# Performance work log

Hardware: AMD Instinct MI355X
Metric: run time of the kernel (lower is better)

## Reference

```python
import jax, jax.numpy as jnp
import numpy as np

NEG_SLOPE = 0.2
EPS = 1e-16


def gatv2_conv(x, src, dst, n_nodes, Wl, Wr, att, bias):
    """GATv2Conv, heads=1, add_self_loops handled by caller via src/dst.
    x: [N, Fin]; src/dst: [E] (message j->i means src=j, dst=i).
    Wl, Wr: [Fin, Fout]; att: [Fout]; bias: [Fout].
    """
    xl = x @ Wl  # [N, Fout] (source transform)
    xr = x @ Wr  # [N, Fout] (target transform)
    # per-edge attention logit: a^T LeakyReLU(xl[j] + xr[i])
    h = xl[src] + xr[dst]                      # [E, Fout]
    e = jax.nn.leaky_relu(h, NEG_SLOPE) @ att  # [E]
    # segment softmax over incoming edges of each dst node
    m = jax.ops.segment_max(e, dst, num_segments=n_nodes)   # [N]
    ex = jnp.exp(e - m[dst])                                 # [E]
    denom = jax.ops.segment_sum(ex, dst, num_segments=n_nodes)  # [N]
    alpha = ex / (denom[dst] + EPS)                          # [E]
    # scatter-aggregate weighted source messages
    out = jax.ops.segment_sum(alpha[:, None] * xl[src], dst, num_segments=n_nodes)
    return out + bias


def glorot(key, shape):
    lim = np.sqrt(6.0 / (shape[0] + shape[1]))
    return jax.random.uniform(key, shape, jnp.float32, -lim, lim)


def setup_inputs() -> dict:
    key = jax.random.key(0)
    ks = jax.random.split(key, 9)
    N, E, Fin, H, Fout = 50000, 800000, 128, 64, 2
    x = jax.random.normal(ks[0], (N, Fin), jnp.float32)
    edge_index = jax.random.randint(ks[1], (2, E), 0, N, jnp.int64)
    return {
        "x": x,
        "edge_index": edge_index,
        "Wl1": glorot(ks[2], (Fin, H)),
        "Wr1": glorot(ks[3], (Fin, H)),
        "att1": glorot(ks[4], (H, 1))[:, 0],
        "b1": jnp.zeros((H,), jnp.float32),
        "Wl2": glorot(ks[5], (H, Fout)),
        "Wr2": glorot(ks[6], (H, Fout)),
        "att2": glorot(ks[7], (Fout, 1))[:, 0],
        "b2": jnp.zeros((Fout,), jnp.float32),
    }


def reference(x, edge_index, Wl1, Wr1, att1, b1, Wl2, Wr2, att2, b2):
    n_nodes = x.shape[0]
    # PyG GATv2Conv adds self-loops by default
    loops = jnp.arange(n_nodes, dtype=edge_index.dtype)
    src = jnp.concatenate([edge_index[0], loops])
    dst = jnp.concatenate([edge_index[1], loops])
    # eval mode: dropout is identity; the initial relu/dropout result is dead code
    h = gatv2_conv(x, src, dst, n_nodes, Wl1, Wr1, att1, b1)
    out = gatv2_conv(h, src, dst, n_nodes, Wl2, Wr2, att2, b2)
    return out
```

## Files before the change

### kernel.cpp

```cpp
#include <hip/hip_runtime.h>
#include <math.h>

#define FIN 128
#define H 64
#define FOUT 2
#define NEG_SLOPE 0.2f
#define EPS 1e-16f

#define SCAN_CHUNK 2048

typedef __attribute__((ext_vector_type(8))) short s8v;
typedef __attribute__((ext_vector_type(4))) float f4v;

__device__ __forceinline__ void load_bs(const int* __restrict__ blocksum, int nscan,
                                        int* bs, int tid){
  if(tid < 64){
    int v = (tid < nscan)? blocksum[tid] : 0;
    int incl = v;
    #pragma unroll
    for(int o=1;o<64;o<<=1){ int u=__shfl_up(incl,o); if(tid>=o) incl+=u; }
    bs[tid] = incl - v;
  }
  __syncthreads();
}

__global__ void k_prep(int* __restrict__ deg, int N, int ZB,
                       const float* __restrict__ Wl, const float* __restrict__ Wr,
                       unsigned short* __restrict__ pWh, unsigned short* __restrict__ pWe){
  int b = blockIdx.x;
  if(b < ZB){
    int i = b*256 + threadIdx.x;
    if(i < N) deg[i] = 0;
    return;
  }
  int idx = (b - ZB)*256 + threadIdx.x;
  int lane = idx & 63;
  int ctk  = idx >> 6;
  int k0   = (ctk & 3) * 32;
  int ct   = ctk >> 2;
  int c    = ct*16 + (lane & 15);
  int kb   = k0 + (lane >> 4)*8;
  const float* Wp = (c < 64) ? (Wl + c) : (Wr + (c - 64));
  #pragma unroll
  for(int j=0;j<8;j++){
    float v = Wp[(size_t)(kb + j)*H];
    unsigned u = __float_as_uint(v);
    unsigned short hb = (unsigned short)(u >> 16);
    float hv = __uint_as_float(((unsigned)hb) << 16);
    float ev = v - hv;
    unsigned short eb = (unsigned short)(__float_as_uint(ev) >> 16);
    pWh[(size_t)idx*8 + j] = hb;
    pWe[(size_t)idx*8 + j] = eb;
  }
}

__global__ __launch_bounds__(256) void k_gemm_mfma(
    const float* __restrict__ x,
    const unsigned short* __restrict__ pWh, const unsigned short* __restrict__ pWe,
    float* __restrict__ xr, unsigned short* __restrict__ xlb, int N){
  int tid = threadIdx.x;
  int lane = tid & 63, wid = tid >> 6;
  int rowbase = blockIdx.x*64 + wid*16;
  int r = lane & 15, g = lane >> 4;

  int arow = rowbase + r; if(arow > N-1) arow = N-1;
  const float* xrow = x + (size_t)arow*FIN;
  int orow = rowbase + r;

  s8v xh[4], xe[4];
  #pragma unroll
  for(int k0=0;k0<4;k0++){
    float4 va = *(const float4*)(xrow + k0*32 + g*8);
    float4 vb = *(const float4*)(xrow + k0*32 + g*8 + 4);
    float xs_[8] = {va.x,va.y,va.z,va.w,vb.x,vb.y,vb.z,vb.w};
    #pragma unroll
    for(int j=0;j<8;j++){
      unsigned u = __float_as_uint(xs_[j]);
      unsigned short hb = (unsigned short)(u >> 16);
      xh[k0][j] = (short)hb;
      float ev = xs_[j] - __uint_as_float(((unsigned)hb) << 16);
      xe[k0][j] = (short)(unsigned short)(__float_as_uint(ev) >> 16);
    }
  }

  #pragma unroll 2
  for(int ct=0;ct<8;ct++){
    f4v a = (f4v){0.f,0.f,0.f,0.f};
    #pragma unroll
    for(int k0=0;k0<4;k0++){
      size_t boff = ((size_t)(ct*4 + k0)*64 + lane)*8;
      s8v wh = *(const s8v*)(pWh + boff);
      s8v we = *(const s8v*)(pWe + boff);
      a = __builtin_amdgcn_mfma_f32_16x16x32_bf16(wh, xh[k0], a, 0,0,0);
      a = __builtin_amdgcn_mfma_f32_16x16x32_bf16(wh, xe[k0], a, 0,0,0);
      a = __builtin_amdgcn_mfma_f32_16x16x32_bf16(we, xh[k0], a, 0,0,0);
    }
    if(orow < N){
      if(ct < 4){
        ushort4 pk;
        unsigned u0 = __float_as_uint(a[0]);
        unsigned u1 = __float_as_uint(a[1]);
        unsigned u2 = __float_as_uint(a[2]);
        unsigned u3 = __float_as_uint(a[3]);
        pk.x = (unsigned short)((u0 + 0x7FFF + ((u0>>16)&1)) >> 16);
        pk.y = (unsigned short)((u1 + 0x7FFF + ((u1>>16)&1)) >> 16);
        pk.z = (unsigned short)((u2 + 0x7FFF + ((u2>>16)&1)) >> 16);
        pk.w = (unsigned short)((u3 + 0x7FFF + ((u3>>16)&1)) >> 16);
        *(ushort4*)(xlb + (size_t)orow*H + ct*16 + g*4) = pk;
      } else {
        *(float4*)(xr + (size_t)orow*H + (ct-4)*16 + g*4) =
            make_float4(a[0],a[1],a[2],a[3]);
      }
    }
  }
}

__global__ void k_degree(const int* __restrict__ ei, int E, int Etot,
                         int* __restrict__ deg, int* __restrict__ rank){
  int i0 = (blockIdx.x*blockDim.x + threadIdx.x)*8;
  if(i0 >= Etot) return;
  if(i0 + 8 <= E && (E & 3) == 0){
    int4 da = *(const int4*)(ei + E + i0);
    int4 db = *(const int4*)(ei + E + i0 + 4);
    int r0 = atomicAdd(&deg[da.x],1);
    int r1 = atomicAdd(&deg[da.y],1);
    int r2 = atomicAdd(&deg[da.z],1);
    int r3 = atomicAdd(&deg[da.w],1);
    int r4 = atomicAdd(&deg[db.x],1);
    int r5 = atomicAdd(&deg[db.y],1);
    int r6 = atomicAdd(&deg[db.z],1);
    int r7 = atomicAdd(&deg[db.w],1);
    *(int4*)(rank + i0)     = make_int4(r0,r1,r2,r3);
    *(int4*)(rank + i0 + 4) = make_int4(r4,r5,r6,r7);
  } else if(i0 >= E && i0 + 8 <= Etot){
    int v = i0 - E;
    int r0 = atomicAdd(&deg[v+0],1);
    int r1 = atomicAdd(&deg[v+1],1);
    int r2 = atomicAdd(&deg[v+2],1);
    int r3 = atomicAdd(&deg[v+3],1);
    int r4 = atomicAdd(&deg[v+4],1);
    int r5 = atomicAdd(&deg[v+5],1);
    int r6 = atomicAdd(&deg[v+6],1);
    int r7 = atomicAdd(&deg[v+7],1);
    *(int4*)(rank + i0)     = make_int4(r0,r1,r2,r3);
    *(int4*)(rank + i0 + 4) = make_int4(r4,r5,r6,r7);
  } else {
    #pragma unroll
    for(int q=0;q<8;q++){
      int i = i0+q; if(i>=Etot) break;
      int dst = (i<E) ? ei[E+i] : (i-E);
      rank[i] = atomicAdd(&deg[dst],1);
    }
  }
}

__global__ __launch_bounds__(256) void k_scan_a(const int* __restrict__ deg, int n,
                                                int* __restrict__ rowptr,
                                                int* __restrict__ blocksum){
  __shared__ int wsum[4];
  int tid = threadIdx.x, lane = tid & 63, wid = tid >> 6;
  int idx = blockIdx.x*SCAN_CHUNK + tid*8;
  int v[8];
  if(idx + 8 <= n){
    int4 a = *(const int4*)(deg + idx);
    int4 b = *(const int4*)(deg + idx + 4);
    v[0]=a.x;v[1]=a.y;v[2]=a.z;v[3]=a.w;v[4]=b.x;v[5]=b.y;v[6]=b.z;v[7]=b.w;
  } else {
    #pragma unroll
    for(int i=0;i<8;i++) v[i] = (idx+i<n)? deg[idx+i] : 0;
  }
  int pre[8]; int st=0;
  #pragma unroll
  for(int i=0;i<8;i++){ pre[i]=st; st+=v[i]; }
  int incl = st;
  #pragma unroll
  for(int o=1;o<64;o<<=1){ int u=__shfl_up(incl,o); if(lane>=o) incl+=u; }
  if(lane==63) wsum[wid]=incl;
  __syncthreads();
  if(tid==0){ int accu=0; for(int i=0;i<4;i++){ int t=wsum[i]; wsum[i]=accu; accu+=t; } }
  __syncthreads();
  int toff = wsum[wid] + incl - st;
  if(idx + 8 <= n){
    int4 o0 = make_int4(toff+pre[0],toff+pre[1],toff+pre[2],toff+pre[3]);
    int4 o1 = make_int4(toff+pre[4],toff+pre[5],toff+pre[6],toff+pre[7]);
    *(int4*)(rowptr+idx)=o0; *(int4*)(rowptr+idx+4)=o1;
  } else {
    #pragma unroll
    for(int i=0;i<8;i++) if(idx+i<n) rowptr[idx+i]=toff+pre[i];
  }
  if(tid==255){
    blocksum[blockIdx.x] = toff + st;
    if(blockIdx.x == gridDim.x-1) rowptr[n] = toff + st;
  }
}

__global__ void k_fill(const int* __restrict__ ei, int E, int Etot,
                       const int* __restrict__ rowptr,
                       const int* __restrict__ blocksum, int nscan,
                       const int* __restrict__ rank, int* __restrict__ csr_src){
  __shared__ int bs[64];
  int tid = threadIdx.x;
  load_bs(blocksum, nscan, bs, tid);
  int i0 = (blockIdx.x*blockDim.x + tid)*8;
  if(i0 >= Etot) return;
  if(i0 + 8 <= E && (E & 3) == 0){
    int4 sa = *(const int4*)(ei + i0);
    int4 sb = *(const int4*)(ei + i0 + 4);
    int4 da = *(const int4*)(ei + E + i0);
    int4 db = *(const int4*)(ei + E + i0 + 4);
    int4 ra = *(const int4*)(rank + i0);
    int4 rb = *(const int4*)(rank + i0 + 4);
    csr_src[rowptr[da.x] + bs[da.x>>11] + ra.x] = sa.x;
    csr_src[rowptr[da.y] + bs[da.y>>11] + ra.y] = sa.y;
    csr_src[rowptr[da.z] + bs[da.z>>11] + ra.z] = sa.z;
    csr_src[rowptr[da.w] + bs[da.w>>11] + ra.w] = sa.w;
    csr_src[rowptr[db.x] + bs[db.x>>11] + rb.x] = sb.x;
    csr_src[rowptr[db.y] + bs[db.y>>11] + rb.y] = sb.y;
    csr_src[rowptr[db.z] + bs[db.z>>11] + rb.z] = sb.z;
    csr_src[rowptr[db.w] + bs[db.w>>11] + rb.w] = sb.w;
  } else if(i0 >= E && i0 + 8 <= Etot){
    int4 ra = *(const int4*)(rank + i0);
    int4 rb = *(const int4*)(rank + i0 + 4);
    int v = i0 - E;
    csr_src[rowptr[v+0] + bs[(v+0)>>11] + ra.x] = v+0;
    csr_src[rowptr[v+1] + bs[(v+1)>>11] + ra.y] = v+1;
    csr_src[rowptr[v+2] + bs[(v+2)>>11] + ra.z] = v+2;
    csr_src[rowptr[v+3] + bs[(v+3)>>11] + ra.w] = v+3;
    csr_src[rowptr[v+4] + bs[(v+4)>>11] + rb.x] = v+4;
    csr_src[rowptr[v+5] + bs[(v+5)>>11] + rb.y] = v+5;
    csr_src[rowptr[v+6] + bs[(v+6)>>11] + rb.z] = v+6;
    csr_src[rowptr[v+7] + bs[(v+7)>>11] + rb.w] = v+7;
  } else {
    #pragma unroll
    for(int q=0;q<8;q++){
      int i = i0+q; if(i>=Etot) break;
      int src, dst;
      if(i<E){ src = ei[i]; dst = ei[E+i]; } else { src = i-E; dst = i-E; }
      csr_src[rowptr[dst] + bs[dst>>11] + rank[i]] = src;
    }
  }
}

__global__ void k_node1f(const int* __restrict__ rowptr, const int* __restrict__ blocksum,
                         int nscan, const int* __restrict__ csr_src,
                         const unsigned short* __restrict__ xlb, const float* __restrict__ xr,
                         const float* __restrict__ att, const float* __restrict__ b1,
                         const float* __restrict__ Wl2, const float* __restrict__ Wr2,
                         float* __restrict__ xl2, float* __restrict__ xr2, int N){
  __shared__ int bs[64];
  int tid = threadIdx.x;
  load_bs(blocksum, nscan, bs, tid);
  int node = blockIdx.x*8 + (tid>>5);
  int half = (tid >> 4) & 1;
  int gl = tid & 15;
  if(node >= N) return;
  int f4 = gl*4;
  float4 attv = *(const float4*)(att + f4);
  float4 xrv  = *(const float4*)(xr + (size_t)node*H + f4);
  int s = rowptr[node]   + bs[node>>11];
  int t = rowptr[node+1] + bs[(node+1)>>11];
  float d = 0.f;
  float ax=0.f, ay=0.f, az=0.f, aw=0.f;

  for(int k = s + half*8; k < t; k += 16){
    int tl = t - 1;
    int ks[8]; float4 xv[8]; float msk[8];
    #pragma unroll
    for(int j=0;j<8;j++){
      int kj = k + j;
      ks[j] = (kj < t) ? kj : tl;
      msk[j] = (kj < t) ? 1.f : 0.f;
    }
    int ss[8];
    #pragma unroll
    for(int j=0;j<8;j++) ss[j] = csr_src[ks[j]];
    #pragma unroll
    for(int j=0;j<8;j++){
      ushort4 uv = *(const ushort4*)(xlb + (size_t)ss[j]*H + f4);
      xv[j].x = __uint_as_float((unsigned)uv.x << 16);
      xv[j].y = __uint_as_float((unsigned)uv.y << 16);
      xv[j].z = __uint_as_float((unsigned)uv.z << 16);
      xv[j].w = __uint_as_float((unsigned)uv.w << 16);
    }
    #pragma unroll
    for(int j=0;j<8;j++){
      float h0 = xv[j].x + xrv.x, h1 = xv[j].y + xrv.y;
      float h2 = xv[j].z + xrv.z, h3 = xv[j].w + xrv.w;
      float l0 = (h0>0.f)? h0 : NEG_SLOPE*h0;
      float l1 = (h1>0.f)? h1 : NEG_SLOPE*h1;
      float l2 = (h2>0.f)? h2 : NEG_SLOPE*h2;
      float l3 = (h3>0.f)? h3 : NEG_SLOPE*h3;
      float e = l0*attv.x + l1*attv.y + l2*attv.z + l3*attv.w;
      #pragma unroll
      for(int o=1;o<16;o<<=1) e += __shfl_xor(e,o);
      float w = msk[j] * __expf(e);
      d  += w;
      ax += w*xv[j].x; ay += w*xv[j].y; az += w*xv[j].z; aw += w*xv[j].w;
    }
  }

  d  += __shfl_xor(d,16);
  ax += __shfl_xor(ax,16); ay += __shfl_xor(ay,16);
  az += __shfl_xor(az,16); aw += __shfl_xor(aw,16);

  float inv = 1.f/(d + EPS);
  float4 bv = *(const float4*)(b1 + f4);
  float h0 = ax*inv + bv.x, h1 = ay*inv + bv.y;
  float h2 = az*inv + bv.z, h3 = aw*inv + bv.w;
  const float* Wp = half ? Wr2 : Wl2;
  float pa = h0*Wp[(f4+0)*FOUT+0] + h1*Wp[(f4+1)*FOUT+0] + h2*Wp[(f4+2)*FOUT+0] + h3*Wp[(f4+3)*FOUT+0];
  float pb = h0*Wp[(f4+0)*FOUT+1] + h1*Wp[(f4+1)*FOUT+1] + h2*Wp[(f4+2)*FOUT+1] + h3*Wp[(f4+3)*FOUT+1];
  #pragma unroll
  for(int o=1;o<16;o<<=1){
    pa += __shfl_xor(pa,o); pb += __shfl_xor(pb,o);
  }
  if(gl==0){
    float2 pv = make_float2(pa,pb);
    if(half==0) *(float2*)(xl2 + node*2) = pv;
    else        *(float2*)(xr2 + node*2) = pv;
  }
}

__global__ void k_node2(const int* __restrict__ rowptr, const int* __restrict__ blocksum,
                        int nscan, const int* __restrict__ csr_src,
                        const float* __restrict__ xl2, const float* __restrict__ xr2,
                        const float* __restrict__ att2, const float* __restrict__ b2,
                        float* __restrict__ out, int N){
  __shared__ int bs[64];
  int tid = threadIdx.x;
  load_bs(blocksum, nscan, bs, tid);
  int node = blockIdx.x*16 + (tid>>4);
  int gl = tid & 15;
  if(node >= N) return;
  int s = rowptr[node]   + bs[node>>11];
  int t = rowptr[node+1] + bs[(node+1)>>11];
  float2 xrv = *(const float2*)(xr2 + node*2);
  float a0 = att2[0], a1 = att2[1];
  float den=0.f, n0=0.f, n1=0.f;
  for(int k=s+gl; k<t; k+=16){
    int src = csr_src[k];
    float2 xs = *(const float2*)(xl2 + src*2);
    float h0 = xs.x + xrv.x, h1 = xs.y + xrv.y;
    float l0 = (h0>0.f)? h0 : NEG_SLOPE*h0;
    float l1 = (h1>0.f)? h1 : NEG_SLOPE*h1;
    float ex = __expf(l0*a0 + l1*a1);
    den += ex; n0 += ex*xs.x; n1 += ex*xs.y;
  }
  #pragma unroll
  for(int o=1;o<16;o<<=1){
    den += __shfl_xor(den,o);
    n0  += __shfl_xor(n0,o);
    n1  += __shfl_xor(n1,o);
  }
  if(gl==0){
    float inv = 1.f/(den + EPS);
    out[node*2+0] = n0*inv + b2[0];
    out[node*2+1] = n1*inv + b2[1];
  }
}

extern "C" void kernel_launch(void* const* d_in, const int* in_sizes, int n_in,
                              void* d_out, int out_size, void* d_ws, size_t ws_size,
                              hipStream_t stream){
  const float* x    = (const float*)d_in[0];
  const int*   ei   = (const int*)d_in[1];
  const float* Wl1  = (const float*)d_in[2];
  const float* Wr1  = (const float*)d_in[3];
  const float* att1 = (const float*)d_in[4];
  const float* b1   = (const float*)d_in[5];
  const float* Wl2  = (const float*)d_in[6];
  const float* Wr2  = (const float*)d_in[7];
  const float* att2 = (const float*)d_in[8];
  const float* b2   = (const float*)d_in[9];
  int N = in_sizes[0]/FIN;
  int E = in_sizes[1]/2;
  int Etot = E + N;
  int nscan = (N + SCAN_CHUNK - 1) / SCAN_CHUNK;
  int noct  = (Etot + 7) / 8;
  int ZB = (N + 255) / 256;
  int GDO = (noct + 255) / 256;

  char* w = (char*)d_ws;
  size_t off = 0;
  auto alloc = [&](size_t bytes)->void*{
    void* p = w + off;
    off = (off + bytes + 255) & ~(size_t)255;
    return p;
  };
  float* xr1     = (float*)alloc((size_t)N*H*4);
  unsigned short* xlb = (unsigned short*)alloc((size_t)N*H*2);
  int*   csr_src = (int*)  alloc((size_t)Etot*4);
  int*   rank    = (int*)  alloc((size_t)Etot*4);
  int*   deg     = (int*)  alloc((size_t)N*4);
  int*   rowptr  = (int*)  alloc((size_t)(N+1)*4);
  int*   blocksum= (int*)  alloc((size_t)64*4);
  float* xl2     = (float*)alloc((size_t)N*2*4);
  float* xr2     = (float*)alloc((size_t)N*2*4);
  unsigned short* pWh = (unsigned short*)alloc((size_t)2048*8*2);
  unsigned short* pWe = (unsigned short*)alloc((size_t)2048*8*2);

  k_prep<<<ZB+8, 256, 0, stream>>>(deg, N, ZB, Wl1, Wr1, pWh, pWe);
  k_gemm_mfma<<<(N+63)/64, 256, 0, stream>>>(x, pWh, pWe, xr1, xlb, N);
  k_degree<<<GDO,256,0,stream>>>(ei, E, Etot, deg, rank);
  k_scan_a<<<nscan,256,0,stream>>>(deg, N, rowptr, blocksum);
  k_fill<<<GDO,256,0,stream>>>(ei, E, Etot, rowptr, blocksum, nscan, rank, csr_src);
  k_node1f<<<(N+7)/8, 256, 0, stream>>>(rowptr, blocksum, nscan, csr_src,
                                        xlb, xr1, att1, b1, Wl2, Wr2, xl2, xr2, N);
  k_node2<<<(N+15)/16, 256, 0, stream>>>(rowptr, blocksum, nscan, csr_src,
                                         xl2, xr2, att2, b2, (float*)d_out, N);
}
```

Baseline: 128.8 us.

## Stripe degree counters into four copies and use one 16-lane group per node

The degree histogram is split into four sub-counters, selected by edge position within each 8-edge chunk, so concurrent atomics on the same destination contend less. The scan kernel turns these into per-stripe exclusive offsets, and the fill kernel adds the stripe offset when placing each source index. Separately, the layer-1 node kernel now gives each node a single 16-lane group instead of two half-groups, which removes the cross-half shuffle reduction and computes both layer-2 projections in that group. The cost is four times the counter memory and zeroing, extra loads in fill, and serial edge processing per node with less parallelism for high-degree nodes.

```diff
diff --git a/kernel.cpp b/kernel.cpp
--- a/kernel.cpp
+++ b/kernel.cpp
@@ -24,13 +24,13 @@
   __syncthreads();
 }
 
-__global__ void k_prep(int* __restrict__ deg, int N, int ZB,
+__global__ void k_prep(int* __restrict__ degs, int N4, int ZB,
                        const float* __restrict__ Wl, const float* __restrict__ Wr,
                        unsigned short* __restrict__ pWh, unsigned short* __restrict__ pWe){
   int b = blockIdx.x;
   if(b < ZB){
     int i = b*256 + threadIdx.x;
-    if(i < N) deg[i] = 0;
+    if(i < N4) degs[i] = 0;
     return;
   }
   int idx = (b - ZB)*256 + threadIdx.x;
@@ -115,33 +115,33 @@
   }
 }
 
-__global__ void k_degree(const int* __restrict__ ei, int E, int Etot,
-                         int* __restrict__ deg, int* __restrict__ rank){
+__global__ void k_degree(const int* __restrict__ ei, int E, int Etot, int N,
+                         int* __restrict__ degs, int* __restrict__ rank){
   int i0 = (blockIdx.x*blockDim.x + threadIdx.x)*8;
   if(i0 >= Etot) return;
-  if(i0 + 8 <= E && (E & 3) == 0){
+  if(i0 + 8 <= E){
     int4 da = *(const int4*)(ei + E + i0);
     int4 db = *(const int4*)(ei + E + i0 + 4);
-    int r0 = atomicAdd(&deg[da.x],1);
-    int r1 = atomicAdd(&deg[da.y],1);
-    int r2 = atomicAdd(&deg[da.z],1);
-    int r3 = atomicAdd(&deg[da.w],1);
-    int r4 = atomicAdd(&deg[db.x],1);
-    int r5 = atomicAdd(&deg[db.y],1);
-    int r6 = atomicAdd(&deg[db.z],1);
-    int r7 = atomicAdd(&deg[db.w],1);
+    int r0 = atomicAdd(&degs[        da.x],1);
+    int r1 = atomicAdd(&degs[        da.y],1);
+    int r2 = atomicAdd(&degs[  N +   da.z],1);
+    int r3 = atomicAdd(&degs[  N +   da.w],1);
+    int r4 = atomicAdd(&degs[2*N +   db.x],1);
+    int r5 = atomicAdd(&degs[2*N +   db.y],1);
+    int r6 = atomicAdd(&degs[3*N +   db.z],1);
+    int r7 = atomicAdd(&degs[3*N +   db.w],1);
     *(int4*)(rank + i0)     = make_int4(r0,r1,r2,r3);
     *(int4*)(rank + i0 + 4) = make_int4(r4,r5,r6,r7);
   } else if(i0 >= E && i0 + 8 <= Etot){
     int v = i0 - E;
-    int r0 = atomicAdd(&deg[v+0],1);
-    int r1 = atomicAdd(&deg[v+1],1);
-    int r2 = atomicAdd(&deg[v+2],1);
-    int r3 = atomicAdd(&deg[v+3],1);
-    int r4 = atomicAdd(&deg[v+4],1);
-    int r5 = atomicAdd(&deg[v+5],1);
-    int r6 = atomicAdd(&deg[v+6],1);
-    int r7 = atomicAdd(&deg[v+7],1);
+    int r0 = atomicAdd(&degs[        v+0],1);
+    int r1 = atomicAdd(&degs[        v+1],1);
+    int r2 = atomicAdd(&degs[  N +   v+2],1);
+    int r3 = atomicAdd(&degs[  N +   v+3],1);
+    int r4 = atomicAdd(&degs[2*N +   v+4],1);
+    int r5 = atomicAdd(&degs[2*N +   v+5],1);
+    int r6 = atomicAdd(&degs[3*N +   v+6],1);
+    int r7 = atomicAdd(&degs[3*N +   v+7],1);
     *(int4*)(rank + i0)     = make_int4(r0,r1,r2,r3);
     *(int4*)(rank + i0 + 4) = make_int4(r4,r5,r6,r7);
   } else {
@@ -149,12 +149,13 @@
     for(int q=0;q<8;q++){
       int i = i0+q; if(i>=Etot) break;
       int dst = (i<E) ? ei[E+i] : (i-E);
-      rank[i] = atomicAdd(&deg[dst],1);
-    }
-  }
-}
-
-__global__ __launch_bounds__(256) void k_scan_a(const int* __restrict__ deg, int n,
+      int s = q >> 1;
+      rank[i] = atomicAdd(&degs[s*N + dst],1);
+    }
+  }
+}
+
+__global__ __launch_bounds__(256) void k_scan_a(int* __restrict__ degs, int n,
                                                 int* __restrict__ rowptr,
                                                 int* __restrict__ blocksum){
   __shared__ int wsum[4];
@@ -162,12 +163,32 @@
   int idx = blockIdx.x*SCAN_CHUNK + tid*8;
   int v[8];
   if(idx + 8 <= n){
-    int4 a = *(const int4*)(deg + idx);
-    int4 b = *(const int4*)(deg + idx + 4);
-    v[0]=a.x;v[1]=a.y;v[2]=a.z;v[3]=a.w;v[4]=b.x;v[5]=b.y;v[6]=b.z;v[7]=b.w;
+    int4 a0 = *(const int4*)(degs + idx),         a1 = *(const int4*)(degs + idx + 4);
+    int4 b0 = *(const int4*)(degs + n + idx),     b1 = *(const int4*)(degs + n + idx + 4);
+    int4 c0 = *(const int4*)(degs + 2*n + idx),   c1 = *(const int4*)(degs + 2*n + idx + 4);
+    int4 e0 = *(const int4*)(degs + 3*n + idx),   e1 = *(const int4*)(degs + 3*n + idx + 4);
+    *(int4*)(degs + n + idx)     = a0;
+    *(int4*)(degs + n + idx + 4) = a1;
+    int4 s20 = make_int4(a0.x+b0.x, a0.y+b0.y, a0.z+b0.z, a0.w+b0.w);
+    int4 s21 = make_int4(a1.x+b1.x, a1.y+b1.y, a1.z+b1.z, a1.w+b1.w);
+    *(int4*)(degs + 2*n + idx)     = s20;
+    *(int4*)(degs + 2*n + idx + 4) = s21;
+    int4 s30 = make_int4(s20.x+c0.x, s20.y+c0.y, s20.z+c0.z, s20.w+c0.w);
+    int4 s31 = make_int4(s21.x+c1.x, s21.y+c1.y, s21.z+c1.z, s21.w+c1.w);
+    *(int4*)(degs + 3*n + idx)     = s30;
+    *(int4*)(degs + 3*n + idx + 4) = s31;
+    v[0]=s30.x+e0.x; v[1]=s30.y+e0.y; v[2]=s30.z+e0.z; v[3]=s30.w+e0.w;
+    v[4]=s31.x+e1.x; v[5]=s31.y+e1.y; v[6]=s31.z+e1.z; v[7]=s31.w+e1.w;
   } else {
     #pragma unroll
-    for(int i=0;i<8;i++) v[i] = (idx+i<n)? deg[idx+i] : 0;
+    for(int i=0;i<8;i++){
+      int p = idx+i;
+      if(p < n){
+        int d0=degs[p], d1=degs[n+p], d2=degs[2*n+p], d3=degs[3*n+p];
+        degs[n+p]=d0; degs[2*n+p]=d0+d1; degs[3*n+p]=d0+d1+d2;
+        v[i]=d0+d1+d2+d3;
+      } else v[i]=0;
+    }
   }
   int pre[8]; int st=0;
   #pragma unroll
@@ -194,49 +215,52 @@
   }
 }
 
-__global__ void k_fill(const int* __restrict__ ei, int E, int Etot,
+__global__ void k_fill(const int* __restrict__ ei, int E, int Etot, int N,
                        const int* __restrict__ rowptr,
                        const int* __restrict__ blocksum, int nscan,
+                       const int* __restrict__ degs,
                        const int* __restrict__ rank, int* __restrict__ csr_src){
   __shared__ int bs[64];
   int tid = threadIdx.x;
   load_bs(blocksum, nscan, bs, tid);
   int i0 = (blockIdx.x*blockDim.x + tid)*8;
   if(i0 >= Etot) return;
-  if(i0 + 8 <= E && (E & 3) == 0){
+  if(i0 + 8 <= E){
     int4 sa = *(const int4*)(ei + i0);
     int4 sb = *(const int4*)(ei + i0 + 4);
     int4 da = *(const int4*)(ei + E + i0);
     int4 db = *(const int4*)(ei + E + i0 + 4);
     int4 ra = *(const int4*)(rank + i0);
     int4 rb = *(const int4*)(rank + i0 + 4);
-    csr_src[rowptr[da.x] + bs[da.x>>11] + ra.x] = sa.x;
-    csr_src[rowptr[da.y] + bs[da.y>>11] + ra.y] = sa.y;
-    csr_src[rowptr[da.z] + bs[da.z>>11] + ra.z] = sa.z;
-    csr_src[rowptr[da.w] + bs[da.w>>11] + ra.w] = sa.w;
-    csr_src[rowptr[db.x] + bs[db.x>>11] + rb.x] = sb.x;
-    csr_src[rowptr[db.y] + bs[db.y>>11] + rb.y] = sb.y;
-    csr_src[rowptr[db.z] + bs[db.z>>11] + rb.z] = sb.z;
-    csr_src[rowptr[db.w] + bs[db.w>>11] + rb.w] = sb.w;
+    csr_src[rowptr[da.x] + bs[da.x>>11] +                   ra.x] = sa.x;
+    csr_src[rowptr[da.y] + bs[da.y>>11] +                   ra.y] = sa.y;
+    csr_src[rowptr[da.z] + bs[da.z>>11] + degs[  N + da.z] + ra.z] = sa.z;
+    csr_src[rowptr[da.w] + bs[da.w>>11] + degs[  N + da.w] + ra.w] = sa.w;
+    csr_src[rowptr[db.x] + bs[db.x>>11] + degs[2*N + db.x] + rb.x] = sb.x;
+    csr_src[rowptr[db.y] + bs[db.y>>11] + degs[2*N + db.y] + rb.y] = sb.y;
+    csr_src[rowptr[db.z] + bs[db.z>>11] + degs[3*N + db.z] + rb.z] = sb.z;
+    csr_src[rowptr[db.w] + bs[db.w>>11] + degs[3*N + db.w] + rb.w] = sb.w;
   } else if(i0 >= E && i0 + 8 <= Etot){
     int4 ra = *(const int4*)(rank + i0);
     int4 rb = *(const int4*)(rank + i0 + 4);
     int v = i0 - E;
-    csr_src[rowptr[v+0] + bs[(v+0)>>11] + ra.x] = v+0;
-    csr_src[rowptr[v+1] + bs[(v+1)>>11] + ra.y] = v+1;
-    csr_src[rowptr[v+2] + bs[(v+2)>>11] + ra.z] = v+2;
-    csr_src[rowptr[v+3] + bs[(v+3)>>11] + ra.w] = v+3;
-    csr_src[rowptr[v+4] + bs[(v+4)>>11] + rb.x] = v+4;
-    csr_src[rowptr[v+5] + bs[(v+5)>>11] + rb.y] = v+5;
-    csr_src[rowptr[v+6] + bs[(v+6)>>11] + rb.z] = v+6;
-    csr_src[rowptr[v+7] + bs[(v+7)>>11] + rb.w] = v+7;
+    csr_src[rowptr[v+0] + bs[(v+0)>>11] +                    ra.x] = v+0;
+    csr_src[rowptr[v+1] + bs[(v+1)>>11] +                    ra.y] = v+1;
+    csr_src[rowptr[v+2] + bs[(v+2)>>11] + degs[  N + (v+2)] + ra.z] = v+2;
+    csr_src[rowptr[v+3] + bs[(v+3)>>11] + degs[  N + (v+3)] + ra.w] = v+3;
+    csr_src[rowptr[v+4] + bs[(v+4)>>11] + degs[2*N + (v+4)] + rb.x] = v+4;
+    csr_src[rowptr[v+5] + bs[(v+5)>>11] + degs[2*N + (v+5)] + rb.y] = v+5;
+    csr_src[rowptr[v+6] + bs[(v+6)>>11] + degs[3*N + (v+6)] + rb.z] = v+6;
+    csr_src[rowptr[v+7] + bs[(v+7)>>11] + degs[3*N + (v+7)] + rb.w] = v+7;
   } else {
     #pragma unroll
     for(int q=0;q<8;q++){
       int i = i0+q; if(i>=Etot) break;
       int src, dst;
       if(i<E){ src = ei[i]; dst = ei[E+i]; } else { src = i-E; dst = i-E; }
-      csr_src[rowptr[dst] + bs[dst>>11] + rank[i]] = src;
+      int s = q >> 1;
+      int so = s ? degs[s*N + dst] : 0;
+      csr_src[rowptr[dst] + bs[dst>>11] + so + rank[i]] = src;
     }
   }
 }
@@ -250,8 +274,7 @@
   __shared__ int bs[64];
   int tid = threadIdx.x;
   load_bs(blocksum, nscan, bs, tid);
-  int node = blockIdx.x*8 + (tid>>5);
-  int half = (tid >> 4) & 1;
+  int node = blockIdx.x*16 + (tid>>4);
   int gl = tid & 15;
   if(node >= N) return;
   int f4 = gl*4;
@@ -262,7 +285,7 @@
   float d = 0.f;
   float ax=0.f, ay=0.f, az=0.f, aw=0.f;
 
-  for(int k = s + half*8; k < t; k += 16){
+  for(int k=s; k<t; k+=8){
     int tl = t - 1;
     int ks[8]; float4 xv[8]; float msk[8];
     #pragma unroll
@@ -299,25 +322,22 @@
     }
   }
 
-  d  += __shfl_xor(d,16);
-  ax += __shfl_xor(ax,16); ay += __shfl_xor(ay,16);
-  az += __shfl_xor(az,16); aw += __shfl_xor(aw,16);
-
   float inv = 1.f/(d + EPS);
   float4 bv = *(const float4*)(b1 + f4);
   float h0 = ax*inv + bv.x, h1 = ay*inv + bv.y;
   float h2 = az*inv + bv.z, h3 = aw*inv + bv.w;
-  const float* Wp = half ? Wr2 : Wl2;
-  float pa = h0*Wp[(f4+0)*FOUT+0] + h1*Wp[(f4+1)*FOUT+0] + h2*Wp[(f4+2)*FOUT+0] + h3*Wp[(f4+3)*FOUT+0];
-  float pb = h0*Wp[(f4+0)*FOUT+1] + h1*Wp[(f4+1)*FOUT+1] + h2*Wp[(f4+2)*FOUT+1] + h3*Wp[(f4+3)*FOUT+1];
+  float p0 = h0*Wl2[(f4+0)*FOUT+0] + h1*Wl2[(f4+1)*FOUT+0] + h2*Wl2[(f4+2)*FOUT+0] + h3*Wl2[(f4+3)*FOUT+0];
+  float p1 = h0*Wl2[(f4+0)*FOUT+1] + h1*Wl2[(f4+1)*FOUT+1] + h2*Wl2[(f4+2)*FOUT+1] + h3*Wl2[(f4+3)*FOUT+1];
+  float p2 = h0*Wr2[(f4+0)*FOUT+0] + h1*Wr2[(f4+1)*FOUT+0] + h2*Wr2[(f4+2)*FOUT+0] + h3*Wr2[(f4+3)*FOUT+0];
+  float p3 = h0*Wr2[(f4+0)*FOUT+1] + h1*Wr2[(f4+1)*FOUT+1] + h2*Wr2[(f4+2)*FOUT+1] + h3*Wr2[(f4+3)*FOUT+1];
   #pragma unroll
   for(int o=1;o<16;o<<=1){
-    pa += __shfl_xor(pa,o); pb += __shfl_xor(pb,o);
+    p0 += __shfl_xor(p0,o); p1 += __shfl_xor(p1,o);
+    p2 += __shfl_xor(p2,o); p3 += __shfl_xor(p3,o);
   }
   if(gl==0){
-    float2 pv = make_float2(pa,pb);
-    if(half==0) *(float2*)(xl2 + node*2) = pv;
-    else        *(float2*)(xr2 + node*2) = pv;
+    *(float2*)(xl2 + node*2) = make_float2(p0,p1);
+    *(float2*)(xr2 + node*2) = make_float2(p2,p3);
   }
 }
 
@@ -377,7 +397,7 @@
   int Etot = E + N;
   int nscan = (N + SCAN_CHUNK - 1) / SCAN_CHUNK;
   int noct  = (Etot + 7) / 8;
-  int ZB = (N + 255) / 256;
+  int ZB = (4*N + 255) / 256;
   int GDO = (noct + 255) / 256;
 
   char* w = (char*)d_ws;
@@ -391,7 +411,7 @@
   unsigned short* xlb = (unsigned short*)alloc((size_t)N*H*2);
   int*   csr_src = (int*)  alloc((size_t)Etot*4);
   int*   rank    = (int*)  alloc((size_t)Etot*4);
-  int*   deg     = (int*)  alloc((size_t)N*4);
+  int*   degs    = (int*)  alloc((size_t)4*N*4);
   int*   rowptr  = (int*)  alloc((size_t)(N+1)*4);
   int*   blocksum= (int*)  alloc((size_t)64*4);
   float* xl2     = (float*)alloc((size_t)N*2*4);
@@ -399,13 +419,13 @@
   unsigned short* pWh = (unsigned short*)alloc((size_t)2048*8*2);
   unsigned short* pWe = (unsigned short*)alloc((size_t)2048*8*2);
 
-  k_prep<<<ZB+8, 256, 0, stream>>>(deg, N, ZB, Wl1, Wr1, pWh, pWe);
+  k_prep<<<ZB+8, 256, 0, stream>>>(degs, 4*N, ZB, Wl1, Wr1, pWh, pWe);
   k_gemm_mfma<<<(N+63)/64, 256, 0, stream>>>(x, pWh, pWe, xr1, xlb, N);
-  k_degree<<<GDO,256,0,stream>>>(ei, E, Etot, deg, rank);
-  k_scan_a<<<nscan,256,0,stream>>>(deg, N, rowptr, blocksum);
-  k_fill<<<GDO,256,0,stream>>>(ei, E, Etot, rowptr, blocksum, nscan, rank, csr_src);
-  k_node1f<<<(N+7)/8, 256, 0, stream>>>(rowptr, blocksum, nscan, csr_src,
-                                        xlb, xr1, att1, b1, Wl2, Wr2, xl2, xr2, N);
+  k_degree<<<GDO,256,0,stream>>>(ei, E, Etot, N, degs, rank);
+  k_scan_a<<<nscan,256,0,stream>>>(degs, N, rowptr, blocksum);
+  k_fill<<<GDO,256,0,stream>>>(ei, E, Etot, N, rowptr, blocksum, nscan, degs, rank, csr_src);
+  k_node1f<<<(N+15)/16, 256, 0, stream>>>(rowptr, blocksum, nscan, csr_src,
+                                          xlb, xr1, att1, b1, Wl2, Wr2, xl2, xr2, N);
   k_node2<<<(N+15)/16, 256, 0, stream>>>(rowptr, blocksum, nscan, csr_src,
                                          xl2, xr2, att2, b2, (float*)d_out, N);
 }
```

Measured after the change: 122.9 us (median of 2 runs). 4.6% less time.
